# Optimization experiments

Measured on AMD Instinct MI355X. Metric: run time of the kernel, lower is better.

The kernel has to match this reference:

```python
import jax, jax.numpy as jnp
import numpy as np

B, T = 256, 64
L, S = 1024, 512          # large / small LSTM cell sizes
NC = 239                  # num classes
EPS = 1e-5                # BatchNorm eps (inference mode, mean=0, var=1)
TAU = 1.0                 # gumbel-softmax temperature


def setup_inputs() -> dict:
    key = jax.random.key(0)
    ks = jax.random.split(key, 12)
    def N(i, shape, s=0.05):
        return jax.random.normal(ks[i], shape, dtype=jnp.float32) * s
    return {
        "x": N(0, (B, T, 2048), 1.0),
        "x_small": N(1, (B, T, 1280), 1.0),
        # proj_mlp: Linear(2048->2048) + BN(2048) [inference] + ReLU
        "W_p": N(2, (2048, 2048)), "b_p": jnp.zeros(2048),
        "g_p": jnp.ones(2048), "be_p": jnp.zeros(2048),
        # small_proj_mlp: Linear(1280->512) + BN(512) + ReLU
        "W_s": N(3, (512, 1280)), "b_s": jnp.zeros(512),
        "g_s": jnp.ones(512), "be_s": jnp.zeros(512),
        # large LSTMCell: input 2048+512 -> hidden L
        "Wih_l": N(4, (4 * L, 2048 + 512)), "Whh_l": N(5, (4 * L, L)),
        "bih_l": jnp.zeros(4 * L), "bhh_l": jnp.zeros(4 * L),
        # small LSTMCell: input 512 -> hidden S
        "Wih_s": N(6, (4 * S, 512)), "Whh_s": N(7, (4 * S, S)),
        "bih_s": jnp.zeros(4 * S), "bhh_s": jnp.zeros(4 * S),
        # gate linear: (512 + 2L) -> 2
        "W_g": N(8, (2, 512 + 2 * L)), "b_g": jnp.zeros(2),
        # classifier: L -> NC
        "W_c": N(9, (NC, L)), "b_c": jnp.zeros(NC),
    }


def _bn_relu(x, gamma, beta):
    # inference BatchNorm1d with running_mean=0, running_var=1
    return jax.nn.relu(x * (gamma / np.sqrt(1.0 + EPS)) + beta)


def _lstm_cell(xin, h, c, Wih, Whh, bih, bhh):
    gates = xin @ Wih.T + bih + h @ Whh.T + bhh
    i, f, g, o = jnp.split(gates, 4, axis=1)
    c2 = jax.nn.sigmoid(f) * c + jax.nn.sigmoid(i) * jnp.tanh(g)
    h2 = jax.nn.sigmoid(o) * jnp.tanh(c2)
    return h2, c2


def reference(x, x_small, W_p, b_p, g_p, be_p, W_s, b_s, g_s, be_s,
              Wih_l, Whh_l, bih_l, bhh_l, Wih_s, Whh_s, bih_s, bhh_s,
              W_g, b_g, W_c, b_c):
    # project all frames at once (time-parallel part of the net)
    feats = _bn_relu(jnp.einsum('bti,oi->bto', x, W_p) + b_p, g_p, be_p)        # [B,T,2048]
    sfeats = _bn_relu(jnp.einsum('bti,oi->bto', x_small, W_s) + b_s, g_s, be_s)  # [B,T,512]

    def step(carry, ft_st):
        h_l, c_l, h_s, c_s = carry
        f_t, s_t = ft_st                                   # [B,2048], [B,512]
        h_s2, c_s2 = _lstm_cell(s_t, h_s, c_s, Wih_s, Whh_s, bih_s, bhh_s)
        # gating on OLD large state
        p = jax.nn.log_softmax(jnp.concatenate([s_t, h_l, c_l], 1) @ W_g.T + b_g, axis=1)
        y_soft = jax.nn.softmax(p / TAU, axis=1)
        y_hard = jax.nn.one_hot(jnp.argmax(y_soft, axis=1), 2, dtype=y_soft.dtype)
        r = y_hard + y_soft - jax.lax.stop_gradient(y_soft)  # straight-through hard sample
        h_ln, c_ln = _lstm_cell(jnp.concatenate([f_t, s_t], 1), h_l, c_l,
                                Wih_l, Whh_l, bih_l, bhh_l)
        ph = jnp.concatenate([h_s2[:, :S], h_l[:, S:L]], 1)  # partial (skip) hidden
        pc = jnp.concatenate([c_s2[:, :S], c_l[:, S:L]], 1)
        h_l2 = r[:, 0:1] * h_ln + r[:, 1:2] * ph
        c_l2 = r[:, 0:1] * c_ln + r[:, 1:2] * pc
        return (h_l2, c_l2, h_s2, c_s2), r

    z_l = jnp.zeros((B, L), jnp.float32)
    z_s = jnp.zeros((B, S), jnp.float32)
    (h_l, c_l, _, _), r_stack = jax.lax.scan(
        step, (z_l, z_l, z_s, z_s),
        (feats.transpose(1, 0, 2), sfeats.transpose(1, 0, 2)))
    logits = h_l @ W_c.T + b_c                             # [B,NC]
    return logits, r_stack                                 # r_stack: [T,B,2]
```

## Files before the change

kernel.cpp:

```cpp
#include <hip/hip_runtime.h>
#include <math.h>


typedef _Float16 f16;
typedef _Float16 f16x4 __attribute__((ext_vector_type(4)));
typedef _Float16 f16x8 __attribute__((ext_vector_type(8)));
typedef float f32x4 __attribute__((ext_vector_type(4)));

__device__ __forceinline__ float sigf(float x) { return 1.0f / (1.0f + expf(-x)); }

__device__ __forceinline__ void gload16(const f16* g, f16* l) {
  __builtin_amdgcn_global_load_lds((const __attribute__((address_space(1))) void*)g,
                                   (__attribute__((address_space(3))) void*)l, 16, 0, 0);
}

__device__ __forceinline__ void cohort_map(int lin, int gA, int gB, int swz,
                                           int& pA, int& pB) {
  if (swz && (gA & 1) == 0 && (gB & 3) == 0) {
    const int xcd = lin & 7;
    const int j = lin >> 3;
    const int pbp = gB >> 2;
    pB = (xcd & 3) * pbp + (j % pbp);
    pA = (xcd >> 2) * (gA >> 1) + (j / pbp);
  } else {
    pB = lin % gB;
    pA = lin / gB;
  }
}

__global__ __launch_bounds__(256) void pack_img(const float* __restrict__ src,
    int C, int KT, int t0, int map, f16* __restrict__ dh, f16* __restrict__ dl,
    int slots)
{
  int gid = blockIdx.x * 256 + threadIdx.x;
  if (gid >= slots) return;
  int lane = gid & 63;
  int j = (gid >> 6) & 7;
  int pk = gid >> 9;
  int p = pk / KT, kt = pk - p * KT;
  int r = p * 128 + j * 16 + (lane & 15);
  int rg = map ? (((r & 255) << 6) + t0 + (r >> 8)) : r;
  int c = kt * 32 + (lane >> 4) * 8;
  const float* s = src + (long long)rg * C + c;
  float4 v0 = *(const float4*)s, v1 = *(const float4*)(s + 4);
  f16x8 h, l;
  h[0]=(f16)v0.x; l[0]=(f16)(v0.x-(float)h[0]);
  h[1]=(f16)v0.y; l[1]=(f16)(v0.y-(float)h[1]);
  h[2]=(f16)v0.z; l[2]=(f16)(v0.z-(float)h[2]);
  h[3]=(f16)v0.w; l[3]=(f16)(v0.w-(float)h[3]);
  h[4]=(f16)v1.x; l[4]=(f16)(v1.x-(float)h[4]);
  h[5]=(f16)v1.y; l[5]=(f16)(v1.y-(float)h[5]);
  h[6]=(f16)v1.z; l[6]=(f16)(v1.z-(float)h[6]);
  h[7]=(f16)v1.w; l[7]=(f16)(v1.w-(float)h[7]);
  *(f16x8*)(dh + (long long)gid * 8) = h;
  *(f16x8*)(dl + (long long)gid * 8) = l;
}

template <int EPI>
__global__ __launch_bounds__(512, 1) void gmm256(
    int gA, int gB, int swz,
    const f16* __restrict__ Ah0, const f16* __restrict__ Al0, int KT0,
    const f16* __restrict__ Ah1, const f16* __restrict__ Al1, int KT1,
    const f16* __restrict__ Bh, const f16* __restrict__ Bl, int KTB,
    float* __restrict__ C, int ldc,
    const float* __restrict__ e0, const float* __restrict__ e1)
{
  __shared__ __align__(16) char smem[131072];
  f16 (*sm)[4][8192] = (f16 (*)[4][8192])smem;
  const int tid = threadIdx.x;
  const int w = tid >> 6, lane = tid & 63;
  const int wr = w >> 2, wc = w & 3;
  const int fr = lane & 15, fq = lane >> 4;
  int pA, pB;
  cohort_map(blockIdx.x, gA, gB, swz, pA, pB);
  const int sarr = w >> 1, shalf = w & 1;

  const int nt = KT0 + KT1;

  auto stage = [&](int buf, int kt) {
    const f16* base;
    if (sarr >= 2) {
      base = ((sarr == 2) ? Bh : Bl) + ((long long)(pB * 2 + shalf) * KTB + kt) * 4096;
    } else if (kt < KT0) {
      base = ((sarr == 0) ? Ah0 : Al0) + ((long long)(pA * 2 + shalf) * KT0 + kt) * 4096;
    } else {
      base = ((sarr == 0) ? Ah1 : Al1) + ((long long)(pA * 2 + shalf) * KT1 + (kt - KT0)) * 4096;
    }
    f16* dst = &sm[buf][sarr][shalf * 4096];
#pragma unroll
    for (int j = 0; j < 8; ++j)
      gload16(base + j * 512 + lane * 8, dst + j * 512);
  };

  f32x4 acc[8][4];
#pragma unroll
  for (int m = 0; m < 8; ++m)
#pragma unroll
    for (int n = 0; n < 4; ++n) acc[m][n] = (f32x4){0.f, 0.f, 0.f, 0.f};

  stage(0, 0);
  __syncthreads();
  int cur = 0;
  for (int kt = 0; kt < nt; ++kt) {
    if (kt + 1 < nt) stage(cur ^ 1, kt + 1);
    f16x8 bh_[4], bl_[4];
#pragma unroll
    for (int n = 0; n < 4; ++n) {
      bh_[n] = *(const f16x8*)&sm[cur][2][(wc * 4 + n) * 512 + lane * 8];
      bl_[n] = *(const f16x8*)&sm[cur][3][(wc * 4 + n) * 512 + lane * 8];
    }
#pragma unroll
    for (int m = 0; m < 8; ++m) {
      f16x8 ah = *(const f16x8*)&sm[cur][0][wr * 4096 + m * 512 + lane * 8];
      f16x8 al = *(const f16x8*)&sm[cur][1][wr * 4096 + m * 512 + lane * 8];
#pragma unroll
      for (int n = 0; n < 4; ++n) {
        acc[m][n] = __builtin_amdgcn_mfma_f32_16x16x32_f16(ah, bh_[n], acc[m][n], 0, 0, 0);
        acc[m][n] = __builtin_amdgcn_mfma_f32_16x16x32_f16(ah, bl_[n], acc[m][n], 0, 0, 0);
        acc[m][n] = __builtin_amdgcn_mfma_f32_16x16x32_f16(al, bh_[n], acc[m][n], 0, 0, 0);
      }
    }
    __syncthreads();
    cur ^= 1;
  }

#pragma unroll
  for (int m = 0; m < 8; ++m) {
#pragma unroll
    for (int n = 0; n < 4; ++n) {
      const int col = pB * 256 + wc * 64 + n * 16 + fr;
      const float add = e0[col] + e1[col];
#pragma unroll
      for (int r = 0; r < 4; ++r) {
        const int row = pA * 256 + wr * 128 + m * 16 + fq * 4 + r;
        C[(long long)row * ldc + col] = acc[m][n][r] + add;
      }
    }
  }
}

template <int EPI>
__device__ __forceinline__ void gcore(
    int pA, int pB,
    const f16* __restrict__ Ah0, const f16* __restrict__ Al0, int KT0,
    const f16* __restrict__ Ah1, const f16* __restrict__ Al1, int KT1,
    const f16* __restrict__ Bh, const f16* __restrict__ Bl, int KTB,
    float* __restrict__ C, int ldc, const float* __restrict__ G,
    f16* __restrict__ Ch, f16* __restrict__ Cl, int KTout,
    const float* __restrict__ e0, const float* __restrict__ e1,
    const float* __restrict__ e2)
{
  constexpr int U = 32;
  constexpr int NU = 8;
  __shared__ __align__(16) f16 smem[2][U * 512];

  const int tid = threadIdx.x;
  const int w = tid >> 6, lane = tid & 63;
  const int wr = w >> 1, wc = w & 1;
  const int fr = lane & 15, fq = lane >> 4;
  const int nt = KT0 + KT1;

  const f16* up[NU];
  auto setptrs = [&](int kt) {
#pragma unroll
    for (int i = 0; i < NU; ++i) {
      const int u = w * NU + i;
      const f16* src;
      if (u < 16) {
        const int j = u & 7;
        const f16* AH = Ah0; const f16* AL = Al0; int KT = KT0, ktl = kt;
        if (KT1 > 0 && kt >= KT0) { AH = Ah1; AL = Al1; KT = KT1; ktl = kt - KT0; }
        src = ((u < 8) ? AH : AL) + (((long long)pA * KT + ktl) * 8 + j) * 512;
      } else {
        const int j = u - 16;
        const f16* IMG = (j < 8) ? Bh : Bl;
        const int jb = j & 7;
        src = IMG + (((long long)pB * KTB + kt) * 8 + jb) * 512;
      }
      up[i] = src + lane * 8;
    }
  };
  auto stage = [&](int buf) {
#pragma unroll
    for (int i = 0; i < NU; ++i) {
      gload16(up[i], &smem[buf][(w * NU + i) * 512]);
      up[i] += 4096;
    }
  };

  f32x4 acc[4][4];
#pragma unroll
  for (int m = 0; m < 4; ++m)
#pragma unroll
    for (int n = 0; n < 4; ++n) acc[m][n] = (f32x4){0.f, 0.f, 0.f, 0.f};

  setptrs(0);
  stage(0);
  __syncthreads();
  int cur = 0;
  for (int kt = 0; kt < nt; ++kt) {
    if (kt + 1 < nt) {
      if (KT1 > 0 && kt + 1 == KT0) setptrs(kt + 1);
      stage(cur ^ 1);
    }
    const f16* sb = smem[cur];
    f16x8 bh_[4], bl_[4];
#pragma unroll
    for (int n = 0; n < 4; ++n) {
      const int jb = wc * 4 + n;
      bh_[n] = *(const f16x8*)&sb[(16 + jb) * 512 + lane * 8];
      bl_[n] = *(const f16x8*)&sb[(24 + jb) * 512 + lane * 8];
    }
#pragma unroll
    for (int m = 0; m < 4; ++m) {
      const int ja = wr * 4 + m;
      f16x8 ah = *(const f16x8*)&sb[ja * 512 + lane * 8];
      f16x8 al = *(const f16x8*)&sb[(8 + ja) * 512 + lane * 8];
#pragma unroll
      for (int n = 0; n < 4; ++n) {
        acc[m][n] = __builtin_amdgcn_mfma_f32_16x16x32_f16(ah, bh_[n], acc[m][n], 0, 0, 0);
        acc[m][n] = __builtin_amdgcn_mfma_f32_16x16x32_f16(ah, bl_[n], acc[m][n], 0, 0, 0);
        acc[m][n] = __builtin_amdgcn_mfma_f32_16x16x32_f16(al, bh_[n], acc[m][n], 0, 0, 0);
      }
    }
    __syncthreads();
    cur ^= 1;
  }

  if constexpr (EPI == 1 || EPI == 2) {
#pragma unroll
    for (int m = 0; m < 4; ++m) {
#pragma unroll
      for (int n = 0; n < 4; ++n) {
        const int col = pB * 128 + wc * 64 + n * 16 + fr;
        const float add = (EPI == 1) ? (e0[col] + e1[col]) : 0.f;
#pragma unroll
        for (int r = 0; r < 4; ++r) {
          const int row = pA * 128 + wr * 64 + m * 16 + fq * 4 + r;
          const long long idx = (long long)row * ldc + col;
          float v = acc[m][n][r] + add;
          if (EPI == 2) v += G[idx];
          C[idx] = v;
        }
      }
    }
  } else {
    float* cb = (float*)smem;
    const int CBLD = 132;
    for (int h = 0; h < 2; ++h) {
      if (wr == h) {
#pragma unroll
        for (int m = 0; m < 4; ++m) {
#pragma unroll
          for (int n = 0; n < 4; ++n) {
            const int colL = wc * 64 + n * 16 + fr;
            const int colG = pB * 128 + colL;
            const float p0 = e0[colG], p1 = e1[colG] * 0.99999500003750f,
                        p2 = e2[colG];
#pragma unroll
            for (int r = 0; r < 4; ++r) {
              const int rq = m * 16 + fq * 4 + r;
              cb[rq * CBLD + colL] = fmaxf((acc[m][n][r] + p0) * p1 + p2, 0.f);
            }
          }
        }
      }
      __syncthreads();
#pragma unroll
      for (int jl = 0; jl < 4; ++jl) {
        const float* s = &cb[(jl * 16 + fr) * CBLD + w * 32 + fq * 8];
        float4 v0 = *(const float4*)s, v1 = *(const float4*)(s + 4);
        float vv[8] = {v0.x, v0.y, v0.z, v0.w, v1.x, v1.y, v1.z, v1.w};
        f16x8 hh, ll;
#pragma unroll
        for (int e = 0; e < 8; ++e) {
          hh[e] = (f16)vv[e]; ll[e] = (f16)(vv[e] - (float)hh[e]);
        }
        const long long o =
            (((long long)pA * KTout + pB * 4 + w) * 8 + (h * 4 + jl)) * 512
            + lane * 8;
        *(f16x8*)(Ch + o) = hh;
        *(f16x8*)(Cl + o) = ll;
      }
      __syncthreads();
    }
  }
}

template <int EPI>
__global__ __launch_bounds__(256) void gmm_k(
    int gA, int gB, int swz,
    const f16* __restrict__ Ah0, const f16* __restrict__ Al0, int KT0,
    const f16* __restrict__ Ah1, const f16* __restrict__ Al1, int KT1,
    const f16* __restrict__ Bh, const f16* __restrict__ Bl, int KTB,
    float* __restrict__ C, int ldc, const float* __restrict__ G,
    f16* __restrict__ Ch, f16* __restrict__ Cl, int KTout,
    const float* __restrict__ e0, const float* __restrict__ e1,
    const float* __restrict__ e2)
{
  int pA, pB;
  cohort_map(blockIdx.x, gA, gB, swz, pA, pB);
  gcore<EPI>(pA, pB, Ah0, Al0, KT0, Ah1, Al1, KT1, Bh, Bl, KTB,
             C, ldc, G, Ch, Cl, KTout, e0, e1, e2);
}

__global__ __launch_bounds__(256) void stepg_k(
    const f16* __restrict__ hlh, const f16* __restrict__ hll,
    const f16* __restrict__ hsh, const f16* __restrict__ hsl,
    const f16* __restrict__ Whlh, const f16* __restrict__ Whll,
    const f16* __restrict__ Whsh, const f16* __restrict__ Whsl,
    const float* __restrict__ Gl, const float* __restrict__ Gs,
    float* __restrict__ gl, float* __restrict__ gs)
{
  const int lin = blockIdx.x;
  const int xc = lin & 7, j = lin >> 3;
  const f16 *Ah, *Al, *Bh, *Bl;
  const float* G; float* C;
  int KT, ldc, pA, pB;
  if (j < 8) {
    pA = j >> 2; pB = xc * 4 + (j & 3);
    Ah = hlh; Al = hll; Bh = Whlh; Bl = Whll; KT = 32; ldc = 4096;
    C = gl; G = Gl;
  } else {
    const int jj = j - 8;
    pA = jj >> 1; pB = xc * 2 + (jj & 1);
    Ah = hsh; Al = hsl; Bh = Whsh; Bl = Whsl; KT = 16; ldc = 2048;
    C = gs; G = Gs;
  }
  gcore<2>(pA, pB, Ah, Al, KT, nullptr, nullptr, 0, Bh, Bl, KT,
           C, ldc, G, nullptr, nullptr, 0, nullptr, nullptr, nullptr);
}

__global__ __launch_bounds__(256) void zs_img_k(const f16* __restrict__ sfh,
    const f16* __restrict__ sfl, const float* __restrict__ Wg,
    float* __restrict__ zs, int t0)
{
  const int wv = threadIdx.x >> 6, lane = threadIdx.x & 63;
  const int rr = blockIdx.x * 4 + wv;
  const int p = rr >> 7, j = (rr >> 4) & 7, fr = rr & 15;
  const int kt = lane >> 2, fq = lane & 3;
  const long long a = (((long long)p * 16 + kt) * 8 + j) * 512 + (fq * 16 + fr) * 8;
  f16x8 h8 = *(const f16x8*)(sfh + a);
  f16x8 l8 = *(const f16x8*)(sfl + a);
  const int k0 = kt * 32 + fq * 8;
  float z0 = 0.f, z1 = 0.f;
#pragma unroll
  for (int i = 0; i < 8; ++i) {
    float s = (float)h8[i] + (float)l8[i];
    z0 += s * Wg[k0 + i]; z1 += s * Wg[2560 + k0 + i];
  }
#pragma unroll
  for (int off = 32; off > 0; off >>= 1) {
    z0 += __shfl_down(z0, off);
    z1 += __shfl_down(z1, off);
  }
  if (lane == 0) {
    const int bt = ((rr & 255) << 6) + t0 + (rr >> 8);
    zs[bt * 2] = z0; zs[bt * 2 + 1] = z1;
  }
}

__global__ __launch_bounds__(256) void step_upd(
    const float* __restrict__ gl, const float* __restrict__ gs,
    const float* __restrict__ hl_o, const float* __restrict__ cl_o,
    const float* __restrict__ cs_o,
    float* __restrict__ hl_n, float* __restrict__ cl_n,
    float* __restrict__ hs_n, float* __restrict__ cs_n,
    f16* __restrict__ hlIh, f16* __restrict__ hlIl,
    f16* __restrict__ hsIh, f16* __restrict__ hsIl,
    const float* __restrict__ zs, const float* __restrict__ Wg,
    const float* __restrict__ bg, float* __restrict__ rout, int t)
{
  const int b = blockIdx.x, tid = threadIdx.x;
  __shared__ float red0[256], red1[256];
  __shared__ float shs[512], scs[512];
  __shared__ float rsh[2];

  const int pb = b >> 7, jb = (b >> 4) & 7, frb = b & 15;

  float4 h4 = *(const float4*)(hl_o + (long long)b * 1024 + tid * 4);
  float4 c4 = *(const float4*)(cl_o + (long long)b * 1024 + tid * 4);
  float4 w0h = *(const float4*)(Wg + 512 + tid * 4);
  float4 w0c = *(const float4*)(Wg + 1536 + tid * 4);
  float4 w1h = *(const float4*)(Wg + 2560 + 512 + tid * 4);
  float4 w1c = *(const float4*)(Wg + 2560 + 1536 + tid * 4);
  red0[tid] = h4.x * w0h.x + h4.y * w0h.y + h4.z * w0h.z + h4.w * w0h.w
            + c4.x * w0c.x + c4.y * w0c.y + c4.z * w0c.z + c4.w * w0c.w;
  red1[tid] = h4.x * w1h.x + h4.y * w1h.y + h4.z * w1h.z + h4.w * w1h.w
            + c4.x * w1c.x + c4.y * w1c.y + c4.z * w1c.z + c4.w * w1c.w;

  {
    const float* gb = gs + (long long)b * 2048;
#pragma unroll
    for (int e = 0; e < 2; ++e) {
      const int n = tid * 2 + e;
      float gi = gb[n], gf = gb[512 + n], gg = gb[1024 + n], go = gb[1536 + n];
      float c2 = sigf(gf) * cs_o[b * 512 + n] + sigf(gi) * tanhf(gg);
      float h2 = sigf(go) * tanhf(c2);
      shs[n] = h2; scs[n] = c2;
      hs_n[b * 512 + n] = h2; cs_n[b * 512 + n] = c2;
      const int kt = n >> 5, fqn = (n >> 3) & 3, en = n & 7;
      const long long o = (((long long)pb * 16 + kt) * 8 + jb) * 512
                        + (fqn * 16 + frb) * 8 + en;
      f16 hh = (f16)h2;
      hsIh[o] = hh; hsIl[o] = (f16)(h2 - (float)hh);
    }
  }
  __syncthreads();
  for (int s = 128; s > 0; s >>= 1) {
    if (tid < s) { red0[tid] += red0[tid + s]; red1[tid] += red1[tid + s]; }
    __syncthreads();
  }
  if (tid == 0) {
    float z0 = red0[0] + zs[(b * 64 + t) * 2 + 0] + bg[0];
    float z1 = red1[0] + zs[(b * 64 + t) * 2 + 1] + bg[1];
    int hard = (z1 > z0) ? 1 : 0;
    rsh[0] = hard ? 0.0f : 1.0f; rsh[1] = hard ? 1.0f : 0.0f;
    rout[b * 2 + 0] = rsh[0]; rout[b * 2 + 1] = rsh[1];
  }
  __syncthreads();
  const float r0 = rsh[0], r1 = rsh[1];

  {
    const float* glb = gl + (long long)b * 4096;
    const int n = tid * 4;
    float4 gi4 = *(const float4*)(glb + n);
    float4 gf4 = *(const float4*)(glb + 1024 + n);
    float4 gg4 = *(const float4*)(glb + 2048 + n);
    float4 go4 = *(const float4*)(glb + 3072 + n);
    float4 co4 = *(const float4*)(cl_o + (long long)b * 1024 + n);
    float4 ho4 = *(const float4*)(hl_o + (long long)b * 1024 + n);
    float gi[4] = {gi4.x, gi4.y, gi4.z, gi4.w};
    float gf[4] = {gf4.x, gf4.y, gf4.z, gf4.w};
    float gg[4] = {gg4.x, gg4.y, gg4.z, gg4.w};
    float go[4] = {go4.x, go4.y, go4.z, go4.w};
    float co[4] = {co4.x, co4.y, co4.z, co4.w};
    float ho[4] = {ho4.x, ho4.y, ho4.z, ho4.w};
    float hv[4], cv[4];
    f16x4 ih, il;
#pragma unroll
    for (int e = 0; e < 4; ++e) {
      float cln = sigf(gf[e]) * co[e] + sigf(gi[e]) * tanhf(gg[e]);
      float hln = sigf(go[e]) * tanhf(cln);
      float ph = (n + e < 512) ? shs[n + e] : ho[e];
      float pc = (n + e < 512) ? scs[n + e] : co[e];
      hv[e] = r0 * hln + r1 * ph;
      cv[e] = r0 * cln + r1 * pc;
      ih[e] = (f16)hv[e]; il[e] = (f16)(hv[e] - (float)ih[e]);
    }
    float4 hw = {hv[0], hv[1], hv[2], hv[3]};
    float4 cw = {cv[0], cv[1], cv[2], cv[3]};
    *(float4*)(hl_n + (long long)b * 1024 + n) = hw;
    *(float4*)(cl_n + (long long)b * 1024 + n) = cw;
    const int kt = n >> 5, fqn = (n >> 3) & 3, en = n & 7;
    const long long o = (((long long)pb * 32 + kt) * 8 + jb) * 512
                      + (fqn * 16 + frb) * 8 + en;
    *(f16x4*)(hlIh + o) = ih;
    *(f16x4*)(hlIl + o) = il;
  }
}

__global__ __launch_bounds__(256) void logits_k(const float* __restrict__ hl,
                                                const float* __restrict__ Wc,
                                                const float* __restrict__ bc,
                                                float* __restrict__ out)
{
  __shared__ float hsd[1024];
  const int b = blockIdx.x, tid = threadIdx.x;
  *(float4*)(hsd + tid * 4) = *(const float4*)(hl + (long long)b * 1024 + tid * 4);
  __syncthreads();
  if (tid < 239) {
    const float* w = Wc + (long long)tid * 1024;
    float s = 0.0f;
    for (int k = 0; k < 1024; k += 4) {
      float4 wv = *(const float4*)(w + k);
      s += hsd[k] * wv.x + hsd[k + 1] * wv.y + hsd[k + 2] * wv.z + hsd[k + 3] * wv.w;
    }
    out[(long long)b * 239 + tid] = s + bc[tid];
  }
}

#define BKK 32
template <int BM, int BN, int TM, int TN, int EPI>
__global__ __launch_bounds__(256) void gemm_nt(
    int M, int N,
    const float* __restrict__ A0, long long as0, const float* __restrict__ B0, long long bs0, int K0,
    const float* __restrict__ A1, long long as1, const float* __restrict__ B1, long long bs1, int K1,
    const float* __restrict__ A2, long long as2, const float* __restrict__ B2, long long bs2, int K2,
    float* __restrict__ C, long long ldc,
    const float* __restrict__ e0, const float* __restrict__ e1, const float* __restrict__ e2)
{
  __shared__ float As[BKK][BM + 4];
  __shared__ float Bs[BKK][BN + 4];
  const int tid = threadIdx.x;
  const int m0 = blockIdx.x * BM;
  const int n0 = blockIdx.y * BN;
  constexpr int C4 = BKK / 4;
  constexpr int RPP = 256 / C4;
  constexpr int APASS = BM / RPP;
  constexpr int BPASS = BN / RPP;
  const int lr = tid / C4;
  const int lc = tid % C4;
  float4 pa[APASS], pb[BPASS];
  const int nt = (K0 + K1 + K2) / BKK;
  auto load = [&](int kt) {
    const int kg = kt * BKK;
    const float* ap; long long as_; const float* bp; long long bs_;
    if (kg < K0)           { ap = A0 + kg;          as_ = as0; bp = B0 + kg;          bs_ = bs0; }
    else if (kg < K0 + K1) { int kl = kg - K0;      ap = A1 + kl; as_ = as1; bp = B1 + kl; bs_ = bs1; }
    else                   { int kl = kg - K0 - K1; ap = A2 + kl; as_ = as2; bp = B2 + kl; bs_ = bs2; }
#pragma unroll
    for (int p = 0; p < APASS; p++) {
      int r = lr + p * RPP;
      pa[p] = *(const float4*)(ap + (long long)(m0 + r) * as_ + lc * 4);
    }
#pragma unroll
    for (int p = 0; p < BPASS; p++) {
      int r = lr + p * RPP;
      pb[p] = *(const float4*)(bp + (long long)(n0 + r) * bs_ + lc * 4);
    }
  };
  const int tx = tid % (BN / TN);
  const int ty = tid / (BN / TN);
  float acc[TM][TN];
#pragma unroll
  for (int i = 0; i < TM; i++)
#pragma unroll
    for (int j = 0; j < TN; j++) acc[i][j] = 0.0f;
  load(0);
  for (int kt = 0; kt < nt; ++kt) {
    __syncthreads();
#pragma unroll
    for (int p = 0; p < APASS; p++) {
      int r = lr + p * RPP;
      As[lc * 4 + 0][r] = pa[p].x; As[lc * 4 + 1][r] = pa[p].y;
      As[lc * 4 + 2][r] = pa[p].z; As[lc * 4 + 3][r] = pa[p].w;
    }
#pragma unroll
    for (int p = 0; p < BPASS; p++) {
      int r = lr + p * RPP;
      Bs[lc * 4 + 0][r] = pb[p].x; Bs[lc * 4 + 1][r] = pb[p].y;
      Bs[lc * 4 + 2][r] = pb[p].z; Bs[lc * 4 + 3][r] = pb[p].w;
    }
    __syncthreads();
    if (kt + 1 < nt) load(kt + 1);
#pragma unroll
    for (int k = 0; k < BKK; k++) {
      float a[TM], bfr[TN];
#pragma unroll
      for (int i = 0; i < TM; i++) a[i] = As[k][ty * TM + i];
#pragma unroll
      for (int j = 0; j < TN; j++) bfr[j] = Bs[k][tx * TN + j];
#pragma unroll
      for (int i = 0; i < TM; i++)
#pragma unroll
        for (int j = 0; j < TN; j++) acc[i][j] += a[i] * bfr[j];
    }
  }
#pragma unroll
  for (int i = 0; i < TM; i++) {
    const int m = m0 + ty * TM + i;
    const int n = n0 + tx * TN;
    float v[TN];
#pragma unroll
    for (int j = 0; j < TN; j++) {
      float a = acc[i][j];
      if (EPI == 0) {
        float s = e1[n + j] * 0.999995f;
        a = (a + e0[n + j]) * s + e2[n + j];
        a = fmaxf(a, 0.0f);
      } else {
        a = a + e0[n + j] + e1[n + j];
      }
      v[j] = a;
    }
    float4 o; o.x = v[0]; o.y = v[1]; o.z = v[2]; o.w = v[3];
    *(float4*)(C + (long long)m * ldc + n) = o;
  }
}

__global__ __launch_bounds__(256) void zs32_k(const float* __restrict__ sf,
                                              const float* __restrict__ Wg,
                                              float* __restrict__ zs)
{
  const int wave = threadIdx.x >> 6, lane = threadIdx.x & 63;
  const int row = blockIdx.x * 4 + wave;
  const float* s = sf + (long long)row * 512 + lane * 8;
  const float* w0 = Wg + lane * 8;
  const float* w1 = Wg + 2560 + lane * 8;
  float4 sa = *(const float4*)s, sb = *(const float4*)(s + 4);
  float4 a0 = *(const float4*)w0, b0 = *(const float4*)(w0 + 4);
  float4 a1 = *(const float4*)w1, b1 = *(const float4*)(w1 + 4);
  float z0 = sa.x * a0.x + sa.y * a0.y + sa.z * a0.z + sa.w * a0.w
           + sb.x * b0.x + sb.y * b0.y + sb.z * b0.z + sb.w * b0.w;
  float z1 = sa.x * a1.x + sa.y * a1.y + sa.z * a1.z + sa.w * a1.w
           + sb.x * b1.x + sb.y * b1.y + sb.z * b1.z + sb.w * b1.w;
#pragma unroll
  for (int off = 32; off > 0; off >>= 1) {
    z0 += __shfl_down(z0, off);
    z1 += __shfl_down(z1, off);
  }
  if (lane == 0) { zs[row * 2] = z0; zs[row * 2 + 1] = z1; }
}

__global__ __launch_bounds__(256) void step_upd32(
    const float* __restrict__ gl, const float* __restrict__ gs,
    const float* __restrict__ hl_o, const float* __restrict__ cl_o,
    const float* __restrict__ cs_o,
    float* __restrict__ hl_n, float* __restrict__ cl_n,
    float* __restrict__ hs_n, float* __restrict__ cs_n,
    const float* __restrict__ zs, const float* __restrict__ Wg,
    const float* __restrict__ bg, float* __restrict__ rout, int t)
{
  const int b = blockIdx.x, tid = threadIdx.x;
  __shared__ float red0[256], red1[256];
  __shared__ float shs[512], scs[512];
  __shared__ float rsh[2];
  float4 h4 = *(const float4*)(hl_o + (long long)b * 1024 + tid * 4);
  float4 c4 = *(const float4*)(cl_o + (long long)b * 1024 + tid * 4);
  float4 w0h = *(const float4*)(Wg + 512 + tid * 4);
  float4 w0c = *(const float4*)(Wg + 1536 + tid * 4);
  float4 w1h = *(const float4*)(Wg + 2560 + 512 + tid * 4);
  float4 w1c = *(const float4*)(Wg + 2560 + 1536 + tid * 4);
  red0[tid] = h4.x * w0h.x + h4.y * w0h.y + h4.z * w0h.z + h4.w * w0h.w
            + c4.x * w0c.x + c4.y * w0c.y + c4.z * w0c.z + c4.w * w0c.w;
  red1[tid] = h4.x * w1h.x + h4.y * w1h.y + h4.z * w1h.z + h4.w * w1h.w
            + c4.x * w1c.x + c4.y * w1c.y + c4.z * w1c.z + c4.w * w1c.w;
  {
    const float* gb = gs + (long long)b * 2048;
#pragma unroll
    for (int e = 0; e < 2; ++e) {
      const int n = tid * 2 + e;
      float gi = gb[n], gf = gb[512 + n], gg = gb[1024 + n], go = gb[1536 + n];
      float c2 = sigf(gf) * cs_o[b * 512 + n] + sigf(gi) * tanhf(gg);
      float h2 = sigf(go) * tanhf(c2);
      shs[n] = h2; scs[n] = c2;
      hs_n[b * 512 + n] = h2; cs_n[b * 512 + n] = c2;
    }
  }
  __syncthreads();
  for (int s = 128; s > 0; s >>= 1) {
    if (tid < s) { red0[tid] += red0[tid + s]; red1[tid] += red1[tid + s]; }
    __syncthreads();
  }
  if (tid == 0) {
    float z0 = red0[0] + zs[(b * 64 + t) * 2 + 0] + bg[0];
    float z1 = red1[0] + zs[(b * 64 + t) * 2 + 1] + bg[1];
    int hard = (z1 > z0) ? 1 : 0;
    rsh[0] = hard ? 0.0f : 1.0f; rsh[1] = hard ? 1.0f : 0.0f;
    rout[b * 2 + 0] = rsh[0]; rout[b * 2 + 1] = rsh[1];
  }
  __syncthreads();
  const float r0 = rsh[0], r1 = rsh[1];
  {
    const float* glb = gl + (long long)b * 4096;
    const int n = tid * 4;
    float4 gi4 = *(const float4*)(glb + n);
    float4 gf4 = *(const float4*)(glb + 1024 + n);
    float4 gg4 = *(const float4*)(glb + 2048 + n);
    float4 go4 = *(const float4*)(glb + 3072 + n);
    float4 co4 = *(const float4*)(cl_o + (long long)b * 1024 + n);
    float4 ho4 = *(const float4*)(hl_o + (long long)b * 1024 + n);
    float gi[4] = {gi4.x, gi4.y, gi4.z, gi4.w};
    float gf[4] = {gf4.x, gf4.y, gf4.z, gf4.w};
    float gg[4] = {gg4.x, gg4.y, gg4.z, gg4.w};
    float go[4] = {go4.x, go4.y, go4.z, go4.w};
    float co[4] = {co4.x, co4.y, co4.z, co4.w};
    float ho[4] = {ho4.x, ho4.y, ho4.z, ho4.w};
    float hv[4], cv[4];
#pragma unroll
    for (int e = 0; e < 4; ++e) {
      float cln = sigf(gf[e]) * co[e] + sigf(gi[e]) * tanhf(gg[e]);
      float hln = sigf(go[e]) * tanhf(cln);
      float ph = (n + e < 512) ? shs[n + e] : ho[e];
      float pc = (n + e < 512) ? scs[n + e] : co[e];
      hv[e] = r0 * hln + r1 * ph;
      cv[e] = r0 * cln + r1 * pc;
    }
    float4 hw = {hv[0], hv[1], hv[2], hv[3]};
    float4 cw = {cv[0], cv[1], cv[2], cv[3]};
    *(float4*)(hl_n + (long long)b * 1024 + n) = hw;
    *(float4*)(cl_n + (long long)b * 1024 + n) = cw;
  }
}

extern "C" void kernel_launch(void* const* d_in, const int* in_sizes, int n_in,
                              void* d_out, int out_size, void* d_ws, size_t ws_size,
                              hipStream_t stream)
{
  const float* x     = (const float*)d_in[0];
  const float* xs    = (const float*)d_in[1];
  const float* W_p   = (const float*)d_in[2];
  const float* b_p   = (const float*)d_in[3];
  const float* g_p   = (const float*)d_in[4];
  const float* be_p  = (const float*)d_in[5];
  const float* W_s   = (const float*)d_in[6];
  const float* b_s   = (const float*)d_in[7];
  const float* g_s   = (const float*)d_in[8];
  const float* be_s  = (const float*)d_in[9];
  const float* Wih_l = (const float*)d_in[10];
  const float* Whh_l = (const float*)d_in[11];
  const float* bih_l = (const float*)d_in[12];
  const float* bhh_l = (const float*)d_in[13];
  const float* Wih_s = (const float*)d_in[14];
  const float* Whh_s = (const float*)d_in[15];
  const float* bih_s = (const float*)d_in[16];
  const float* bhh_s = (const float*)d_in[17];
  const float* W_g   = (const float*)d_in[18];
  const float* b_g   = (const float*)d_in[19];
  const float* W_c   = (const float*)d_in[20];
  const float* b_c   = (const float*)d_in[21];
  float* out = (float*)d_out;
  float* r_out = out + 61184;

  const int BT = 16384;
  const size_t FIXEDB = 100794368ULL;
  const size_t CHUNKB = 12320768ULL;
  int Tp = 0;
  for (int T = 64; T >= 1; T >>= 1)
    if (FIXEDB + CHUNKB * (size_t)T + 65536 <= ws_size) { Tp = T; break; }

  if (Tp > 0) {
    char* base = (char*)d_ws;
    size_t off = 0;
    auto alloc = [&](size_t n) { void* p = base + off; off += (n + 255) & ~255ULL; return p; };
    f16* WpI[2]  = {(f16*)alloc(8388608),  (f16*)alloc(8388608)};
    f16* WsI[2]  = {(f16*)alloc(1310720),  (f16*)alloc(1310720)};
    f16* WilI[2] = {(f16*)alloc(20971520), (f16*)alloc(20971520)};
    f16* WisI[2] = {(f16*)alloc(2097152),  (f16*)alloc(2097152)};
    f16* WhlI[2] = {(f16*)alloc(8388608),  (f16*)alloc(8388608)};
    f16* WhsI[2] = {(f16*)alloc(2097152),  (f16*)alloc(2097152)};
    f16* hlI[2] = {(f16*)alloc(524288), (f16*)alloc(524288)};
    f16* hsI[2] = {(f16*)alloc(262144), (f16*)alloc(262144)};
    float* zs  = (float*)alloc(131072);
    float* hl[2] = {(float*)alloc(1048576), (float*)alloc(1048576)};
    float* cl[2] = {(float*)alloc(1048576), (float*)alloc(1048576)};
    float* hsb[2] = {(float*)alloc(524288), (float*)alloc(524288)};
    float* csb[2] = {(float*)alloc(524288), (float*)alloc(524288)};
    float* gates_l = (float*)alloc(4194304);
    float* gates_s = (float*)alloc(2097152);
    f16* xI[2]  = {(f16*)alloc(1048576ULL * Tp), (f16*)alloc(1048576ULL * Tp)};
    f16* xsI[2] = {(f16*)alloc(655360ULL * Tp),  (f16*)alloc(655360ULL * Tp)};
    f16* feI[2] = {(f16*)alloc(1048576ULL * Tp), (f16*)alloc(1048576ULL * Tp)};
    f16* sfI[2] = {(f16*)alloc(262144ULL * Tp),  (f16*)alloc(262144ULL * Tp)};
    float* GxlC = (float*)alloc(4194304ULL * Tp);
    float* GxsC = (float*)alloc(2097152ULL * Tp);

    pack_img<<<2048, 256, 0, stream>>>(W_p,   2048, 64, 0, 0, WpI[0],  WpI[1],  524288);
    pack_img<<<320,  256, 0, stream>>>(W_s,   1280, 40, 0, 0, WsI[0],  WsI[1],  81920);
    pack_img<<<5120, 256, 0, stream>>>(Wih_l, 2560, 80, 0, 0, WilI[0], WilI[1], 1310720);
    pack_img<<<512,  256, 0, stream>>>(Wih_s, 512,  16, 0, 0, WisI[0], WisI[1], 131072);
    pack_img<<<2048, 256, 0, stream>>>(Whh_l, 1024, 32, 0, 0, WhlI[0], WhlI[1], 524288);
    pack_img<<<512,  256, 0, stream>>>(Whh_s, 512,  16, 0, 0, WhsI[0], WhsI[1], 131072);

    hipMemsetAsync(hl[0], 0, 1048576, stream);
    hipMemsetAsync(cl[0], 0, 1048576, stream);
    hipMemsetAsync(hsb[0], 0, 524288, stream);
    hipMemsetAsync(csb[0], 0, 524288, stream);
    hipMemsetAsync(hlI[0], 0, 524288, stream);
    hipMemsetAsync(hlI[1], 0, 524288, stream);
    hipMemsetAsync(hsI[0], 0, 262144, stream);
    hipMemsetAsync(hsI[1], 0, 262144, stream);

    const int rows = 256 * Tp;
    const int gA1 = rows / 128;
    const int gA2 = rows / 256;
    for (int t0 = 0; t0 < 64; t0 += Tp) {
      pack_img<<<rows * 2048 / 8 / 256, 256, 0, stream>>>(
          x, 2048, 64, t0, 1, xI[0], xI[1], rows * 256);
      pack_img<<<rows * 1280 / 8 / 256, 256, 0, stream>>>(
          xs, 1280, 40, t0, 1, xsI[0], xsI[1], rows * 160);
      gmm_k<0><<<gA1 * 4, 256, 0, stream>>>(
          gA1, 4, 1,
          xsI[0], xsI[1], 40, nullptr, nullptr, 0,
          WsI[0], WsI[1], 40,
          nullptr, 0, nullptr, sfI[0], sfI[1], 16, b_s, g_s, be_s);
      zs_img_k<<<rows / 4, 256, 0, stream>>>(sfI[0], sfI[1], W_g, zs, t0);
      gmm_k<0><<<gA1 * 16, 256, 0, stream>>>(
          gA1, 16, 1,
          xI[0], xI[1], 64, nullptr, nullptr, 0,
          WpI[0], WpI[1], 64,
          nullptr, 0, nullptr, feI[0], feI[1], 64, b_p, g_p, be_p);
      gmm256<1><<<gA2 * 16, 512, 0, stream>>>(
          gA2, 16, 1,
          feI[0], feI[1], 64, sfI[0], sfI[1], 16,
          WilI[0], WilI[1], 80,
          GxlC, 4096, bih_l, bhh_l);
      gmm_k<1><<<gA1 * 16, 256, 0, stream>>>(
          gA1, 16, 1,
          sfI[0], sfI[1], 16, nullptr, nullptr, 0,
          WisI[0], WisI[1], 16,
          GxsC, 2048, nullptr, nullptr, nullptr, 0, bih_s, bhh_s, nullptr);

      for (int tt = 0; tt < Tp; ++tt) {
        const int t = t0 + tt;
        const int o = t & 1, nw = o ^ 1;
        stepg_k<<<96, 256, 0, stream>>>(
            hlI[0], hlI[1], hsI[0], hsI[1],
            WhlI[0], WhlI[1], WhsI[0], WhsI[1],
            GxlC + (long long)tt * 256 * 4096, GxsC + (long long)tt * 256 * 2048,
            gates_l, gates_s);
        step_upd<<<256, 256, 0, stream>>>(
            gates_l, gates_s, hl[o], cl[o], csb[o],
            hl[nw], cl[nw], hsb[nw], csb[nw],
            hlI[0], hlI[1], hsI[0], hsI[1],
            zs, W_g, b_g, r_out + (long long)t * 512, t);
      }
    }
    logits_k<<<256, 256, 0, stream>>>(hl[0], W_c, b_c, out);
    return;
  }

  float* ws = (float*)d_ws;
  size_t offf = 0;
  auto allocf = [&](size_t n) { float* p = ws + offf; offf += n; return p; };
  float* feats   = allocf((size_t)BT * 2048);
  float* sfeats  = allocf((size_t)BT * 512);
  float* zs      = allocf((size_t)BT * 2);
  float* gates_l = allocf((size_t)256 * 4096);
  float* gates_s = allocf((size_t)256 * 2048);
  float* hl[2] = { allocf(256 * 1024), allocf(256 * 1024) };
  float* cl[2] = { allocf(256 * 1024), allocf(256 * 1024) };
  float* hsb[2] = { allocf(256 * 512),  allocf(256 * 512) };
  float* csb[2] = { allocf(256 * 512),  allocf(256 * 512) };

  hipMemsetAsync(hl[0], 0, 256 * 1024 * sizeof(float), stream);
  hipMemsetAsync(cl[0], 0, 256 * 1024 * sizeof(float), stream);
  hipMemsetAsync(hsb[0], 0, 256 * 512 * sizeof(float), stream);
  hipMemsetAsync(csb[0], 0, 256 * 512 * sizeof(float), stream);

  gemm_nt<128, 64, 8, 4, 0><<<dim3(BT / 128, 2048 / 64), 256, 0, stream>>>(
      BT, 2048, x, 2048, W_p, 2048, 2048,
      nullptr, 0, nullptr, 0, 0, nullptr, 0, nullptr, 0, 0,
      feats, 2048, b_p, g_p, be_p);
  gemm_nt<128, 64, 8, 4, 0><<<dim3(BT / 128, 512 / 64), 256, 0, stream>>>(
      BT, 512, xs, 1280, W_s, 1280, 1280,
      nullptr, 0, nullptr, 0, 0, nullptr, 0, nullptr, 0, 0,
      sfeats, 512, b_s, g_s, be_s);
  zs32_k<<<BT / 4, 256, 0, stream>>>(sfeats, W_g, zs);

  for (int t = 0; t < 64; ++t) {
    const int o = t & 1, nw = o ^ 1;
    gemm_nt<64, 64, 4, 4, 1><<<dim3(4, 2048 / 64), 256, 0, stream>>>(
        256, 2048, sfeats + (long long)t * 512, 64LL * 512, Wih_s, 512, 512,
        hsb[o], 512, Whh_s, 512, 512, nullptr, 0, nullptr, 0, 0,
        gates_s, 2048, bih_s, bhh_s, nullptr);
    gemm_nt<64, 64, 4, 4, 1><<<dim3(4, 4096 / 64), 256, 0, stream>>>(
        256, 4096, feats + (long long)t * 2048, 64LL * 2048, Wih_l, 2560, 2048,
        sfeats + (long long)t * 512, 64LL * 512, Wih_l + 2048, 2560, 512,
        hl[o], 1024, Whh_l, 1024, 1024,
        gates_l, 4096, bih_l, bhh_l, nullptr);
    step_upd32<<<256, 256, 0, stream>>>(
        gates_l, gates_s, hl[o], cl[o], csb[o],
        hl[nw], cl[nw], hsb[nw], csb[nw],
        zs, W_g, b_g, r_out + (long long)t * 512, t);
  }
  logits_k<<<256, 256, 0, stream>>>(hl[0], W_c, b_c, out);
}
```

Baseline: 4.043 ms.

## Move projection GEMMs to 256x256 tiles and merge independent launches

The time-parallel projection GEMMs (small proj, large proj, small-LSTM input gates) move from 128x128 tiles to the 256x256 512-thread core, which gains a BN+ReLU epilogue that writes the hi/lo fp16 image through shared memory in four quarters. The large-proj and small-gate GEMMs are fused into one launch, and the two input pack kernels are merged into one. This aims to raise operand reuse per tile and cut launch count. In exchange, grids get smaller and the small-proj launch has only a few blocks, so occupancy drops on those GEMMs.

```diff
diff --git a/kernel.cpp b/kernel.cpp
--- a/kernel.cpp
+++ b/kernel.cpp
@@ -28,12 +28,10 @@
   }
 }
 
-__global__ __launch_bounds__(256) void pack_img(const float* __restrict__ src,
+__device__ __forceinline__ void pack_body(const float* __restrict__ src,
     int C, int KT, int t0, int map, f16* __restrict__ dh, f16* __restrict__ dl,
-    int slots)
-{
-  int gid = blockIdx.x * 256 + threadIdx.x;
-  if (gid >= slots) return;
+    int gid)
+{
   int lane = gid & 63;
   int j = (gid >> 6) & 7;
   int pk = gid >> 9;
@@ -56,23 +54,44 @@
   *(f16x8*)(dl + (long long)gid * 8) = l;
 }
 
+__global__ __launch_bounds__(256) void pack_img(const float* __restrict__ src,
+    int C, int KT, int t0, int map, f16* __restrict__ dh, f16* __restrict__ dl,
+    int slots)
+{
+  int gid = blockIdx.x * 256 + threadIdx.x;
+  if (gid >= slots) return;
+  pack_body(src, C, KT, t0, map, dh, dl, gid);
+}
+
+__global__ __launch_bounds__(256) void pack2_k(int bx,
+    const float* __restrict__ x, const float* __restrict__ xs, int t0,
+    f16* __restrict__ xh, f16* __restrict__ xl,
+    f16* __restrict__ xsh, f16* __restrict__ xsl)
+{
+  if ((int)blockIdx.x < bx) {
+    int gid = blockIdx.x * 256 + threadIdx.x;
+    pack_body(x, 2048, 64, t0, 1, xh, xl, gid);
+  } else {
+    int gid = (blockIdx.x - bx) * 256 + threadIdx.x;
+    pack_body(xs, 1280, 40, t0, 1, xsh, xsl, gid);
+  }
+}
+
 template <int EPI>
-__global__ __launch_bounds__(512, 1) void gmm256(
-    int gA, int gB, int swz,
+__device__ __forceinline__ void gcore256(char* smem, int pA, int pB,
     const f16* __restrict__ Ah0, const f16* __restrict__ Al0, int KT0,
     const f16* __restrict__ Ah1, const f16* __restrict__ Al1, int KT1,
     const f16* __restrict__ Bh, const f16* __restrict__ Bl, int KTB,
     float* __restrict__ C, int ldc,
-    const float* __restrict__ e0, const float* __restrict__ e1)
-{
-  __shared__ __align__(16) char smem[131072];
+    f16* __restrict__ Ch, f16* __restrict__ Cl, int KTout,
+    const float* __restrict__ e0, const float* __restrict__ e1,
+    const float* __restrict__ e2)
+{
   f16 (*sm)[4][8192] = (f16 (*)[4][8192])smem;
   const int tid = threadIdx.x;
   const int w = tid >> 6, lane = tid & 63;
   const int wr = w >> 2, wc = w & 3;
   const int fr = lane & 15, fq = lane >> 4;
-  int pA, pB;
-  cohort_map(blockIdx.x, gA, gB, swz, pA, pB);
   const int sarr = w >> 1, shalf = w & 1;
 
   const int nt = KT0 + KT1;
@@ -124,184 +143,195 @@
     cur ^= 1;
   }
 
-#pragma unroll
-  for (int m = 0; m < 8; ++m) {
-#pragma unroll
-    for (int n = 0; n < 4; ++n) {
-      const int col = pB * 256 + wc * 64 + n * 16 + fr;
-      const float add = e0[col] + e1[col];
-#pragma unroll
-      for (int r = 0; r < 4; ++r) {
-        const int row = pA * 256 + wr * 128 + m * 16 + fq * 4 + r;
-        C[(long long)row * ldc + col] = acc[m][n][r] + add;
-      }
-    }
-  }
-}
-
-template <int EPI>
-__device__ __forceinline__ void gcore(
-    int pA, int pB,
-    const f16* __restrict__ Ah0, const f16* __restrict__ Al0, int KT0,
-    const f16* __restrict__ Ah1, const f16* __restrict__ Al1, int KT1,
-    const f16* __restrict__ Bh, const f16* __restrict__ Bl, int KTB,
-    float* __restrict__ C, int ldc, const float* __restrict__ G,
-    f16* __restrict__ Ch, f16* __restrict__ Cl, int KTout,
-    const float* __restrict__ e0, const float* __restrict__ e1,
-    const float* __restrict__ e2)
-{
-  constexpr int U = 32;
-  constexpr int NU = 8;
-  __shared__ __align__(16) f16 smem[2][U * 512];
-
-  const int tid = threadIdx.x;
-  const int w = tid >> 6, lane = tid & 63;
-  const int wr = w >> 1, wc = w & 1;
-  const int fr = lane & 15, fq = lane >> 4;
-  const int nt = KT0 + KT1;
-
-  const f16* up[NU];
-  auto setptrs = [&](int kt) {
-#pragma unroll
-    for (int i = 0; i < NU; ++i) {
-      const int u = w * NU + i;
-      const f16* src;
-      if (u < 16) {
-        const int j = u & 7;
-        const f16* AH = Ah0; const f16* AL = Al0; int KT = KT0, ktl = kt;
-        if (KT1 > 0 && kt >= KT0) { AH = Ah1; AL = Al1; KT = KT1; ktl = kt - KT0; }
-        src = ((u < 8) ? AH : AL) + (((long long)pA * KT + ktl) * 8 + j) * 512;
-      } else {
-        const int j = u - 16;
-        const f16* IMG = (j < 8) ? Bh : Bl;
-        const int jb = j & 7;
-        src = IMG + (((long long)pB * KTB + kt) * 8 + jb) * 512;
-      }
-      up[i] = src + lane * 8;
-    }
-  };
-  auto stage = [&](int buf) {
-#pragma unroll
-    for (int i = 0; i < NU; ++i) {
-      gload16(up[i], &smem[buf][(w * NU + i) * 512]);
-      up[i] += 4096;
-    }
-  };
-
-  f32x4 acc[4][4];
-#pragma unroll
-  for (int m = 0; m < 4; ++m)
-#pragma unroll
-    for (int n = 0; n < 4; ++n) acc[m][n] = (f32x4){0.f, 0.f, 0.f, 0.f};
-
-  setptrs(0);
-  stage(0);
-  __syncthreads();
-  int cur = 0;
-  for (int kt = 0; kt < nt; ++kt) {
-    if (kt + 1 < nt) {
-      if (KT1 > 0 && kt + 1 == KT0) setptrs(kt + 1);
-      stage(cur ^ 1);
-    }
-    const f16* sb = smem[cur];
-    f16x8 bh_[4], bl_[4];
-#pragma unroll
-    for (int n = 0; n < 4; ++n) {
-      const int jb = wc * 4 + n;
-      bh_[n] = *(const f16x8*)&sb[(16 + jb) * 512 + lane * 8];
-      bl_[n] = *(const f16x8*)&sb[(24 + jb) * 512 + lane * 8];
-    }
-#pragma unroll
-    for (int m = 0; m < 4; ++m) {
-      const int ja = wr * 4 + m;
-      f16x8 ah = *(const f16x8*)&sb[ja * 512 + lane * 8];
-      f16x8 al = *(const f16x8*)&sb[(8 + ja) * 512 + lane * 8];
+  if constexpr (EPI == 1) {
+#pragma unroll
+    for (int m = 0; m < 8; ++m) {
 #pragma unroll
       for (int n = 0; n < 4; ++n) {
-        acc[m][n] = __builtin_amdgcn_mfma_f32_16x16x32_f16(ah, bh_[n], acc[m][n], 0, 0, 0);
-        acc[m][n] = __builtin_amdgcn_mfma_f32_16x16x32_f16(ah, bl_[n], acc[m][n], 0, 0, 0);
-        acc[m][n] = __builtin_amdgcn_mfma_f32_16x16x32_f16(al, bh_[n], acc[m][n], 0, 0, 0);
-      }
-    }
-    __syncthreads();
-    cur ^= 1;
-  }
-
-  if constexpr (EPI == 1 || EPI == 2) {
-#pragma unroll
-    for (int m = 0; m < 4; ++m) {
-#pragma unroll
-      for (int n = 0; n < 4; ++n) {
-        const int col = pB * 128 + wc * 64 + n * 16 + fr;
-        const float add = (EPI == 1) ? (e0[col] + e1[col]) : 0.f;
+        const int col = pB * 256 + wc * 64 + n * 16 + fr;
+        const float add = e0[col] + e1[col];
 #pragma unroll
         for (int r = 0; r < 4; ++r) {
-          const int row = pA * 128 + wr * 64 + m * 16 + fq * 4 + r;
-          const long long idx = (long long)row * ldc + col;
-          float v = acc[m][n][r] + add;
-          if (EPI == 2) v += G[idx];
-          C[idx] = v;
+          const int row = pA * 256 + wr * 128 + m * 16 + fq * 4 + r;
+          C[(long long)row * ldc + col] = acc[m][n][r] + add;
         }
       }
     }
   } else {
     float* cb = (float*)smem;
-    const int CBLD = 132;
-    for (int h = 0; h < 2; ++h) {
-      if (wr == h) {
-#pragma unroll
-        for (int m = 0; m < 4; ++m) {
+    const int CBLD = 260;
+    for (int q = 0; q < 4; ++q) {
+      __syncthreads();
+      if (wr == (q >> 1)) {
+#pragma unroll
+        for (int mm = 0; mm < 4; ++mm) {
+          const int m = (q & 1) * 4 + mm;
 #pragma unroll
           for (int n = 0; n < 4; ++n) {
             const int colL = wc * 64 + n * 16 + fr;
-            const int colG = pB * 128 + colL;
-            const float p0 = e0[colG], p1 = e1[colG] * 0.99999500003750f,
-                        p2 = e2[colG];
+            const int colG = pB * 256 + colL;
+            const float p0 = e0[colG], p1 = e1[colG] * 0.99999500003750f, p2 = e2[colG];
 #pragma unroll
             for (int r = 0; r < 4; ++r) {
-              const int rq = m * 16 + fq * 4 + r;
+              const int rq = mm * 16 + fq * 4 + r;
               cb[rq * CBLD + colL] = fmaxf((acc[m][n][r] + p0) * p1 + p2, 0.f);
             }
           }
         }
       }
       __syncthreads();
-#pragma unroll
-      for (int jl = 0; jl < 4; ++jl) {
-        const float* s = &cb[(jl * 16 + fr) * CBLD + w * 32 + fq * 8];
+      const int ktl = w;
+      const int p_out = pA * 2 + (q >> 1);
+#pragma unroll
+      for (int jp = 0; jp < 4; ++jp) {
+        const int rL = jp * 16 + fr;
+        const float* s = &cb[rL * CBLD + ktl * 32 + fq * 8];
         float4 v0 = *(const float4*)s, v1 = *(const float4*)(s + 4);
         float vv[8] = {v0.x, v0.y, v0.z, v0.w, v1.x, v1.y, v1.z, v1.w};
-        f16x8 hh, ll;
+        f16x8 h, l;
 #pragma unroll
         for (int e = 0; e < 8; ++e) {
-          hh[e] = (f16)vv[e]; ll[e] = (f16)(vv[e] - (float)hh[e]);
+          h[e] = (f16)vv[e]; l[e] = (f16)(vv[e] - (float)h[e]);
         }
+        const int j_img = (q & 1) * 4 + jp;
         const long long o =
-            (((long long)pA * KTout + pB * 4 + w) * 8 + (h * 4 + jl)) * 512
-            + lane * 8;
-        *(f16x8*)(Ch + o) = hh;
-        *(f16x8*)(Cl + o) = ll;
+            (((long long)p_out * KTout + (pB * 8 + ktl)) * 8 + j_img) * 512 + lane * 8;
+        *(f16x8*)(Ch + o) = h;
+        *(f16x8*)(Cl + o) = l;
       }
-      __syncthreads();
     }
   }
 }
 
 template <int EPI>
-__global__ __launch_bounds__(256) void gmm_k(
+__global__ __launch_bounds__(512, 1) void gmm256w(
     int gA, int gB, int swz,
     const f16* __restrict__ Ah0, const f16* __restrict__ Al0, int KT0,
     const f16* __restrict__ Ah1, const f16* __restrict__ Al1, int KT1,
     const f16* __restrict__ Bh, const f16* __restrict__ Bl, int KTB,
-    float* __restrict__ C, int ldc, const float* __restrict__ G,
+    float* __restrict__ C, int ldc,
     f16* __restrict__ Ch, f16* __restrict__ Cl, int KTout,
     const float* __restrict__ e0, const float* __restrict__ e1,
     const float* __restrict__ e2)
 {
+  __shared__ __align__(16) char smem[131072];
   int pA, pB;
   cohort_map(blockIdx.x, gA, gB, swz, pA, pB);
-  gcore<EPI>(pA, pB, Ah0, Al0, KT0, Ah1, Al1, KT1, Bh, Bl, KTB,
-             C, ldc, G, Ch, Cl, KTout, e0, e1, e2);
+  gcore256<EPI>(smem, pA, pB, Ah0, Al0, KT0, Ah1, Al1, KT1, Bh, Bl, KTB,
+                C, ldc, Ch, Cl, KTout, e0, e1, e2);
+}
+
+__global__ __launch_bounds__(512, 1) void fegxs_k(int gA,
+    const f16* __restrict__ xIh, const f16* __restrict__ xIl,
+    const f16* __restrict__ WpIh, const f16* __restrict__ WpIl,
+    f16* __restrict__ feIh, f16* __restrict__ feIl,
+    const float* __restrict__ b_p, const float* __restrict__ g_p,
+    const float* __restrict__ be_p,
+    const f16* __restrict__ sfIh, const f16* __restrict__ sfIl,
+    const f16* __restrict__ WisIh, const f16* __restrict__ WisIl,
+    float* __restrict__ GxsC,
+    const float* __restrict__ bih_s, const float* __restrict__ bhh_s)
+{
+  __shared__ __align__(16) char smem[131072];
+  const int half = gA * 8;
+  if ((int)blockIdx.x < half) {
+    const int lin = blockIdx.x;
+    gcore256<0>(smem, lin >> 3, lin & 7,
+                xIh, xIl, 64, nullptr, nullptr, 0, WpIh, WpIl, 64,
+                nullptr, 0, feIh, feIl, 64, b_p, g_p, be_p);
+  } else {
+    const int lin = blockIdx.x - half;
+    gcore256<1>(smem, lin >> 3, lin & 7,
+                sfIh, sfIl, 16, nullptr, nullptr, 0, WisIh, WisIl, 16,
+                GxsC, 2048, nullptr, nullptr, 0, bih_s, bhh_s, nullptr);
+  }
+}
+
+__device__ __forceinline__ void gcore_step(
+    int pA, int pB,
+    const f16* __restrict__ Ah0, const f16* __restrict__ Al0, int KT0,
+    const f16* __restrict__ Bh, const f16* __restrict__ Bl, int KTB,
+    float* __restrict__ C, int ldc, const float* __restrict__ G)
+{
+  constexpr int NU = 8;
+  __shared__ __align__(16) f16 smem[2][32 * 512];
+
+  const int tid = threadIdx.x;
+  const int w = tid >> 6, lane = tid & 63;
+  const int wr = w >> 1, wc = w & 1;
+  const int fr = lane & 15, fq = lane >> 4;
+
+  const f16* up[NU];
+#pragma unroll
+  for (int i = 0; i < NU; ++i) {
+    const int u = w * NU + i;
+    const f16* src;
+    if (u < 16) {
+      const int j = u & 7;
+      src = ((u < 8) ? Ah0 : Al0) + (((long long)pA * KT0) * 8 + j) * 512;
+    } else {
+      const int j = u - 16;
+      const f16* IMG = (j < 8) ? Bh : Bl;
+      src = IMG + (((long long)pB * KTB) * 8 + (j & 7)) * 512;
+    }
+    up[i] = src + lane * 8;
+  }
+  auto stage = [&](int buf) {
+#pragma unroll
+    for (int i = 0; i < NU; ++i) {
+      gload16(up[i], &smem[buf][(w * NU + i) * 512]);
+      up[i] += 4096;
+    }
+  };
+
+  f32x4 acc[4][4];
+#pragma unroll
+  for (int m = 0; m < 4; ++m)
+#pragma unroll
+    for (int n = 0; n < 4; ++n) acc[m][n] = (f32x4){0.f, 0.f, 0.f, 0.f};
+
+  stage(0);
+  __syncthreads();
+  int cur = 0;
+  for (int kt = 0; kt < KT0; ++kt) {
+    if (kt + 1 < KT0) stage(cur ^ 1);
+    const f16* sb = smem[cur];
+    f16x8 bh_[4], bl_[4];
+#pragma unroll
+    for (int n = 0; n < 4; ++n) {
+      const int jb = wc * 4 + n;
+      bh_[n] = *(const f16x8*)&sb[(16 + jb) * 512 + lane * 8];
+      bl_[n] = *(const f16x8*)&sb[(24 + jb) * 512 + lane * 8];
+    }
+#pragma unroll
+    for (int m = 0; m < 4; ++m) {
+      const int ja = wr * 4 + m;
+      f16x8 ah = *(const f16x8*)&sb[ja * 512 + lane * 8];
+      f16x8 al = *(const f16x8*)&sb[(8 + ja) * 512 + lane * 8];
+#pragma unroll
+      for (int n = 0; n < 4; ++n) {
+        acc[m][n] = __builtin_amdgcn_mfma_f32_16x16x32_f16(ah, bh_[n], acc[m][n], 0, 0, 0);
+        acc[m][n] = __builtin_amdgcn_mfma_f32_16x16x32_f16(ah, bl_[n], acc[m][n], 0, 0, 0);
+        acc[m][n] = __builtin_amdgcn_mfma_f32_16x16x32_f16(al, bh_[n], acc[m][n], 0, 0, 0);
+      }
+    }
+    __syncthreads();
+    cur ^= 1;
+  }
+
+#pragma unroll
+  for (int m = 0; m < 4; ++m) {
+#pragma unroll
+    for (int n = 0; n < 4; ++n) {
+      const int col = pB * 128 + wc * 64 + n * 16 + fr;
+#pragma unroll
+      for (int r = 0; r < 4; ++r) {
+        const int row = pA * 128 + wr * 64 + m * 16 + fq * 4 + r;
+        const long long idx = (long long)row * ldc + col;
+        C[idx] = acc[m][n][r] + G[idx];
+      }
+    }
+  }
 }
 
 __global__ __launch_bounds__(256) void stepg_k(
@@ -314,21 +344,14 @@
 {
   const int lin = blockIdx.x;
   const int xc = lin & 7, j = lin >> 3;
-  const f16 *Ah, *Al, *Bh, *Bl;
-  const float* G; float* C;
-  int KT, ldc, pA, pB;
   if (j < 8) {
-    pA = j >> 2; pB = xc * 4 + (j & 3);
-    Ah = hlh; Al = hll; Bh = Whlh; Bl = Whll; KT = 32; ldc = 4096;
-    C = gl; G = Gl;
+    gcore_step(j >> 2, xc * 4 + (j & 3), hlh, hll, 32, Whlh, Whll, 32,
+               gl, 4096, Gl);
   } else {
     const int jj = j - 8;
-    pA = jj >> 1; pB = xc * 2 + (jj & 1);
-    Ah = hsh; Al = hsl; Bh = Whsh; Bl = Whsl; KT = 16; ldc = 2048;
-    C = gs; G = Gs;
-  }
-  gcore<2>(pA, pB, Ah, Al, KT, nullptr, nullptr, 0, Bh, Bl, KT,
-           C, ldc, G, nullptr, nullptr, 0, nullptr, nullptr, nullptr);
+    gcore_step(jj >> 1, xc * 2 + (jj & 1), hsh, hsl, 16, Whsh, Whsl, 16,
+               gs, 2048, Gs);
+  }
 }
 
 __global__ __launch_bounds__(256) void zs_img_k(const f16* __restrict__ sfh,
@@ -763,34 +786,26 @@
     hipMemsetAsync(hsI[1], 0, 262144, stream);
 
     const int rows = 256 * Tp;
-    const int gA1 = rows / 128;
-    const int gA2 = rows / 256;
+    const int gA2 = Tp;
+    const int bx = rows;
     for (int t0 = 0; t0 < 64; t0 += Tp) {
-      pack_img<<<rows * 2048 / 8 / 256, 256, 0, stream>>>(
-          x, 2048, 64, t0, 1, xI[0], xI[1], rows * 256);
-      pack_img<<<rows * 1280 / 8 / 256, 256, 0, stream>>>(
-          xs, 1280, 40, t0, 1, xsI[0], xsI[1], rows * 160);
-      gmm_k<0><<<gA1 * 4, 256, 0, stream>>>(
-          gA1, 4, 1,
+      pack2_k<<<bx + rows * 5 / 8, 256, 0, stream>>>(
+          bx, x, xs, t0, xI[0], xI[1], xsI[0], xsI[1]);
+      gmm256w<0><<<gA2 * 2, 512, 0, stream>>>(
+          gA2, 2, 0,
           xsI[0], xsI[1], 40, nullptr, nullptr, 0,
           WsI[0], WsI[1], 40,
-          nullptr, 0, nullptr, sfI[0], sfI[1], 16, b_s, g_s, be_s);
+          nullptr, 0, sfI[0], sfI[1], 16, b_s, g_s, be_s);
       zs_img_k<<<rows / 4, 256, 0, stream>>>(sfI[0], sfI[1], W_g, zs, t0);
-      gmm_k<0><<<gA1 * 16, 256, 0, stream>>>(
-          gA1, 16, 1,
-          xI[0], xI[1], 64, nullptr, nullptr, 0,
-          WpI[0], WpI[1], 64,
-          nullptr, 0, nullptr, feI[0], feI[1], 64, b_p, g_p, be_p);
-      gmm256<1><<<gA2 * 16, 512, 0, stream>>>(
+      fegxs_k<<<gA2 * 16, 512, 0, stream>>>(
+          gA2,
+          xI[0], xI[1], WpI[0], WpI[1], feI[0], feI[1], b_p, g_p, be_p,
+          sfI[0], sfI[1], WisI[0], WisI[1], GxsC, bih_s, bhh_s);
+      gmm256w<1><<<gA2 * 16, 512, 0, stream>>>(
           gA2, 16, 1,
           feI[0], feI[1], 64, sfI[0], sfI[1], 16,
           WilI[0], WilI[1], 80,
-          GxlC, 4096, bih_l, bhh_l);
-      gmm_k<1><<<gA1 * 16, 256, 0, stream>>>(
-          gA1, 16, 1,
-          sfI[0], sfI[1], 16, nullptr, nullptr, 0,
-          WisI[0], WisI[1], 16,
-          GxsC, 2048, nullptr, nullptr, nullptr, 0, bih_s, bhh_s, nullptr);
+          GxlC, 4096, nullptr, nullptr, 0, bih_l, bhh_l, nullptr);
 
       for (int tt = 0; tt < Tp; ++tt) {
         const int t = t0 + tt;
```

Result: slower. 4.148 ms (+2.6%).
